# Kernel tuning notes

Hardware: AMD Instinct MI355X
Metric: run time of the kernel (lower is better)

Reference implementation:

```python
import jax, jax.numpy as jnp
import numpy as np

B, H, SQ, SKV, D = 4, 16, 2048, 2048, 128
SCALE = float(np.sqrt(D))  # scale_factor passed to forward; q_k is divided by it


def setup_inputs() -> dict:
    key = jax.random.key(0)
    kq, kk, kv = jax.random.split(key, 3)
    q = jax.random.normal(kq, (B, H, SQ, D), dtype=jnp.float32)
    k = jax.random.normal(kk, (B, H, SKV, D), dtype=jnp.float32)
    v = jax.random.normal(kv, (B, H, SKV, D), dtype=jnp.float32)
    return {"q": q, "k": k, "v": v}


def reference(q, k, v):
    # q_k = q @ k^T, divided by scale_factor
    scores = jnp.einsum("bhqd,bhkd->bhqk", q, k) / SCALE  # [B,H,Sq,Skv]
    attn = jax.nn.softmax(scores, axis=-1)
    # dropout(p=0.1) is identity in eval/inference mode
    out = jnp.einsum("bhqk,bhkd->bhqd", attn, v)  # [B,H,Sq,D]
    return out
```

## Files before the change

### kernel.cpp

```cpp
#include <hip/hip_runtime.h>
#include <hip/hip_bf16.h>

#define B_ 4
#define H_ 16
#define SQ 2048
#define SKV 2048
#define D_ 128
#define BH (B_*H_)
#define BM 128
#define BN 64
#define NITER (SKV/BN)

typedef __attribute__((ext_vector_type(8))) short bf16x8;
typedef __attribute__((ext_vector_type(4))) float f32x4;

__device__ inline unsigned short f2bf(float f) {
    union { float f; unsigned u; } x{f};
    unsigned r = x.u + 0x7fffu + ((x.u >> 16) & 1u);
    return (unsigned short)(r >> 16);
}

#if defined(__has_builtin) && __has_builtin(__builtin_amdgcn_cvt_pk_bf16_f32)
#define PKBF16(a,b) ({ auto _r = __builtin_amdgcn_cvt_pk_bf16_f32((a),(b)); \
                       unsigned _u; __builtin_memcpy(&_u, &_r, 4); _u; })
#else
#define PKBF16(a,b) ((unsigned)f2bf(a) | ((unsigned)f2bf(b) << 16))
#endif

__device__ inline void gl_lds16(const short* g, short* l) {
    __builtin_amdgcn_global_load_lds((const __attribute__((address_space(1))) unsigned*)g,
                                     (__attribute__((address_space(3))) unsigned*)l,
                                     16, 0, 0);
}

__global__ __launch_bounds__(256) void prep(const float* __restrict__ kin,
                                            const float* __restrict__ vin,
                                            short* __restrict__ kbf,
                                            short* __restrict__ vtg) {
    __shared__ short tile[64 * 136];
    int bx = blockIdx.x, tid = threadIdx.x;
    if (bx < 8192) {
        const float4* s = (const float4*)kin;
        uint2* d = (uint2*)kbf;
        int i = bx * 256 + tid;
        const int HALF = (BH * SKV * D_ / 4) / 2;
#pragma unroll
        for (int h = 0; h < 2; ++h) {
            int j = i + h * HALF;
            float4 a = s[j];
            d[j] = make_uint2(PKBF16(a.x, a.y), PKBF16(a.z, a.w));
        }
    } else {
        int bx2 = bx - 8192;
        int bh = bx2 >> 5;
        int t0 = (bx2 & 31) * 64;
        {
            int r = tid >> 4, cg = tid & 15;
#pragma unroll
            for (int s = 0; s < 4; ++s) {
                int rr = r + s * 16;
                const float* p = vin + ((size_t)bh * SKV + t0 + rr) * D_ + cg * 8;
                float4 a = *(const float4*)p;
                float4 b = *(const float4*)(p + 4);
                union { unsigned u[4]; bf16x8 v; } f;
                f.u[0] = PKBF16(a.x, a.y); f.u[1] = PKBF16(a.z, a.w);
                f.u[2] = PKBF16(b.x, b.y); f.u[3] = PKBF16(b.z, b.w);
                *(bf16x8*)&tile[rr * 136 + cg * 8] = f.v;
            }
        }
        __syncthreads();
        {
            int d = tid >> 1, h2 = tid & 1;
#pragma unroll
            for (int s = 0; s < 4; ++s) {
                int kv = h2 * 32 + s * 8;
                union { short u[8]; uint4 q; } o;
#pragma unroll
                for (int j = 0; j < 8; ++j) o.u[j] = tile[(kv + j) * 136 + d];
                *(uint4*)(vtg + ((size_t)bh * D_ + d) * SKV + t0 + kv) = o.q;
            }
        }
    }
}

__global__ __launch_bounds__(256, 3) void fa_kernel(const float* __restrict__ q,
                                                    const short* __restrict__ kbf,
                                                    const short* __restrict__ vtg,
                                                    float* __restrict__ out) {
    __shared__ short Ksh[64 * 128];
    __shared__ short Vsh[128 * 64];
    __shared__ short Psh[4 * 32 * 72];

    const int tid = threadIdx.x;
    const int wave = tid >> 6;
    const int lane = tid & 63;
    const int l16 = lane & 15;
    const int quad = lane >> 4;

    const int bx = blockIdx.x;
    const int qt = bx & 15;
    const int bh = bx >> 4;
    const int qrow0 = qt * BM + wave * 32;

    const float cscale = 1.4426950408889634f * 0.08838834764831845f;

    bf16x8 qf[2][4];
#pragma unroll
    for (int mt = 0; mt < 2; ++mt) {
        int row = qrow0 + mt * 16 + l16;
        const float* qp = q + ((size_t)bh * SQ + row) * D_ + quad * 8;
#pragma unroll
        for (int ks = 0; ks < 4; ++ks) {
            const float* p = qp + ks * 32;
            float4 a = *(const float4*)p;
            float4 b = *(const float4*)(p + 4);
            union { unsigned u[4]; bf16x8 v; } f;
            f.u[0] = PKBF16(a.x * cscale, a.y * cscale);
            f.u[1] = PKBF16(a.z * cscale, a.w * cscale);
            f.u[2] = PKBF16(b.x * cscale, b.y * cscale);
            f.u[3] = PKBF16(b.z * cscale, b.w * cscale);
            qf[mt][ks] = f.v;
        }
    }

    f32x4 oacc[8][2];
#pragma unroll
    for (int dt = 0; dt < 8; ++dt)
#pragma unroll
        for (int mt = 0; mt < 2; ++mt) oacc[dt][mt] = (f32x4)0.f;
    float lsum[2] = {0.f, 0.f};

    const short* kbase = kbf + (size_t)bh * SKV * D_;
    const short* vbase = vtg + (size_t)bh * D_ * SKV;
    const int krow0 = wave * 4 + (lane >> 4);
    const int kc8 = (lane & 15) ^ krow0;
    const short* kg = kbase + krow0 * 128 + kc8 * 8;
    short* kl = Ksh + wave * 512;
    const int vd0 = wave * 8 + (lane >> 3);
    const int vc = (lane & 7) ^ (lane >> 3);
    const short* vg = vbase + (size_t)vd0 * SKV + vc * 8;
    short* vl = Vsh + wave * 512;

    short* const pwav = Psh + wave * 2304;

    for (int it = 0; it < NITER; ++it) {
        __syncthreads();
#pragma unroll
        for (int s = 0; s < 4; ++s) {
            gl_lds16(kg + s * 2048, kl + s * 2048);
            gl_lds16(vg + (size_t)s * 32 * SKV, vl + s * 2048);
        }
        kg += BN * D_;
        vg += BN;
        __syncthreads();

        f32x4 sacc[4][2];
#pragma unroll
        for (int kt = 0; kt < 4; ++kt) {
            sacc[kt][0] = (f32x4)0.f; sacc[kt][1] = (f32x4)0.f;
        }
#pragma unroll
        for (int kt = 0; kt < 4; ++kt)
#pragma unroll
            for (int ks = 0; ks < 4; ++ks) {
                bf16x8 kf = *(const bf16x8*)&Ksh[(kt * 16 + l16) * 128 + (((ks * 4 + quad) ^ l16) << 3)];
                sacc[kt][0] = __builtin_amdgcn_mfma_f32_16x16x32_bf16(kf, qf[0][ks], sacc[kt][0], 0, 0, 0);
                sacc[kt][1] = __builtin_amdgcn_mfma_f32_16x16x32_bf16(kf, qf[1][ks], sacc[kt][1], 0, 0, 0);
            }

#pragma unroll
        for (int mt = 0; mt < 2; ++mt) {
            short* pw = pwav + (mt * 16 + l16) * 72;
#pragma unroll
            for (int kt = 0; kt < 4; ++kt) {
                float p0 = __builtin_amdgcn_exp2f(sacc[kt][mt][0]);
                float p1 = __builtin_amdgcn_exp2f(sacc[kt][mt][1]);
                float p2 = __builtin_amdgcn_exp2f(sacc[kt][mt][2]);
                float p3 = __builtin_amdgcn_exp2f(sacc[kt][mt][3]);
                lsum[mt] += (p0 + p1) + (p2 + p3);
                *(uint2*)(pw + kt * 16 + quad * 4) = make_uint2(PKBF16(p0, p1), PKBF16(p2, p3));
            }
        }

#pragma unroll
        for (int ks = 0; ks < 2; ++ks) {
            bf16x8 pa0 = *(const bf16x8*)(pwav + l16 * 72 + ks * 32 + quad * 8);
            bf16x8 pa1 = *(const bf16x8*)(pwav + (16 + l16) * 72 + ks * 32 + quad * 8);
#pragma unroll
            for (int dt = 0; dt < 8; ++dt) {
                bf16x8 vf = *(const bf16x8*)&Vsh[(dt * 16 + l16) * 64 + ((((ks * 4 + quad) ^ (l16 & 7))) << 3)];
                oacc[dt][0] = __builtin_amdgcn_mfma_f32_16x16x32_bf16(vf, pa0, oacc[dt][0], 0, 0, 0);
                oacc[dt][1] = __builtin_amdgcn_mfma_f32_16x16x32_bf16(vf, pa1, oacc[dt][1], 0, 0, 0);
            }
        }
    }

#pragma unroll
    for (int mt = 0; mt < 2; ++mt) {
        lsum[mt] += __shfl_xor(lsum[mt], 16);
        lsum[mt] += __shfl_xor(lsum[mt], 32);
    }
    const float rl[2] = {1.0f / lsum[0], 1.0f / lsum[1]};
#pragma unroll
    for (int mt = 0; mt < 2; ++mt) {
        float* op = out + ((size_t)bh * SQ + qrow0 + mt * 16 + l16) * D_ + quad * 4;
#pragma unroll
        for (int dt = 0; dt < 8; ++dt) {
            f32x4 v = oacc[dt][mt] * rl[mt];
            *(f32x4*)(op + dt * 16) = v;
        }
    }
}

extern "C" void kernel_launch(void* const* d_in, const int* in_sizes, int n_in,
                              void* d_out, int out_size, void* d_ws, size_t ws_size,
                              hipStream_t stream) {
    const float* q = (const float*)d_in[0];
    const float* k = (const float*)d_in[1];
    const float* v = (const float*)d_in[2];
    float* out = (float*)d_out;

    short* kbf = (short*)d_ws;
    short* vtg = kbf + (size_t)BH * SKV * D_;

    prep<<<8192 + 2048, 256, 0, stream>>>(k, v, kbf, vtg);
    fa_kernel<<<BH * (SQ / BM), 256, 0, stream>>>(q, kbf, vtg, out);
}
```

Baseline: 372.5 us.

## Double-buffer K/V tiles in LDS with BN=32 to overlap loads and MFMA

Halves the KV tile width to 32 and allocates two LDS buffers for K and V. The async global-to-LDS load of the next tile is issued before computing on the current one, so memory latency can overlap the QK^T, exp and PV MFMA work. The K/V address swizzles and the P scratch pitch are adapted to the narrower tile. The prep kernel's V transpose store also gets a new thread-to-data mapping. The cost is twice as many iterations and barriers per tile of work, plus fewer MFMAs between synchronisations.

```diff
diff --git a/kernel.cpp b/kernel.cpp
--- a/kernel.cpp
+++ b/kernel.cpp
@@ -8,7 +8,7 @@
 #define D_ 128
 #define BH (B_*H_)
 #define BM 128
-#define BN 64
+#define BN 32
 #define NITER (SKV/BN)
 
 typedef __attribute__((ext_vector_type(8))) short bf16x8;
@@ -70,14 +70,15 @@
         }
         __syncthreads();
         {
-            int d = tid >> 1, h2 = tid & 1;
+            int row = tid >> 3;
+            int c8 = tid & 7;
 #pragma unroll
             for (int s = 0; s < 4; ++s) {
-                int kv = h2 * 32 + s * 8;
+                int d = row + s * 32;
                 union { short u[8]; uint4 q; } o;
 #pragma unroll
-                for (int j = 0; j < 8; ++j) o.u[j] = tile[(kv + j) * 136 + d];
-                *(uint4*)(vtg + ((size_t)bh * D_ + d) * SKV + t0 + kv) = o.q;
+                for (int j = 0; j < 8; ++j) o.u[j] = tile[(c8 * 8 + j) * 136 + d];
+                *(uint4*)(vtg + ((size_t)bh * D_ + d) * SKV + t0 + c8 * 8) = o.q;
             }
         }
     }
@@ -87,9 +88,9 @@
                                                     const short* __restrict__ kbf,
                                                     const short* __restrict__ vtg,
                                                     float* __restrict__ out) {
-    __shared__ short Ksh[64 * 128];
-    __shared__ short Vsh[128 * 64];
-    __shared__ short Psh[4 * 32 * 72];
+    __shared__ short Ksh[2 * 32 * 128];
+    __shared__ short Vsh[2 * 128 * 32];
+    __shared__ short Psh[4 * 32 * 40];
 
     const int tid = threadIdx.x;
     const int wave = tid >> 6;
@@ -135,44 +136,41 @@
     const int krow0 = wave * 4 + (lane >> 4);
     const int kc8 = (lane & 15) ^ krow0;
     const short* kg = kbase + krow0 * 128 + kc8 * 8;
-    short* kl = Ksh + wave * 512;
-    const int vd0 = wave * 8 + (lane >> 3);
-    const int vc = (lane & 7) ^ (lane >> 3);
+    short* const klbase = Ksh + wave * 512;
+    const int vd0 = wave * 16 + (lane >> 2);
+    const int vc = (lane & 3) ^ ((lane >> 2) & 3);
     const short* vg = vbase + (size_t)vd0 * SKV + vc * 8;
-    short* vl = Vsh + wave * 512;
-
-    short* const pwav = Psh + wave * 2304;
-
-    for (int it = 0; it < NITER; ++it) {
-        __syncthreads();
-#pragma unroll
-        for (int s = 0; s < 4; ++s) {
-            gl_lds16(kg + s * 2048, kl + s * 2048);
-            gl_lds16(vg + (size_t)s * 32 * SKV, vl + s * 2048);
-        }
-        kg += BN * D_;
-        vg += BN;
-        __syncthreads();
-
-        f32x4 sacc[4][2];
-#pragma unroll
-        for (int kt = 0; kt < 4; ++kt) {
-            sacc[kt][0] = (f32x4)0.f; sacc[kt][1] = (f32x4)0.f;
-        }
-#pragma unroll
-        for (int kt = 0; kt < 4; ++kt)
+    short* const vlbase = Vsh + wave * 512;
+
+    short* const pwav = Psh + wave * 1280;
+
+    auto stage = [&](int it, int bufo) {
+        const short* kgi = kg + it * (BN * D_);
+        const short* vgi = vg + it * BN;
+#pragma unroll
+        for (int s = 0; s < 2; ++s) {
+            gl_lds16(kgi + s * 2048, klbase + bufo + s * 2048);
+            gl_lds16(vgi + (size_t)s * 64 * SKV, vlbase + bufo + s * 2048);
+        }
+    };
+
+    auto compute = [&](int bufo) {
+        f32x4 sacc[2][2];
+#pragma unroll
+        for (int kt = 0; kt < 2; ++kt) { sacc[kt][0] = (f32x4)0.f; sacc[kt][1] = (f32x4)0.f; }
+#pragma unroll
+        for (int kt = 0; kt < 2; ++kt)
 #pragma unroll
             for (int ks = 0; ks < 4; ++ks) {
-                bf16x8 kf = *(const bf16x8*)&Ksh[(kt * 16 + l16) * 128 + (((ks * 4 + quad) ^ l16) << 3)];
+                bf16x8 kf = *(const bf16x8*)&Ksh[bufo + (kt * 16 + l16) * 128 + (((ks * 4 + quad) ^ l16) << 3)];
                 sacc[kt][0] = __builtin_amdgcn_mfma_f32_16x16x32_bf16(kf, qf[0][ks], sacc[kt][0], 0, 0, 0);
                 sacc[kt][1] = __builtin_amdgcn_mfma_f32_16x16x32_bf16(kf, qf[1][ks], sacc[kt][1], 0, 0, 0);
             }
-
 #pragma unroll
         for (int mt = 0; mt < 2; ++mt) {
-            short* pw = pwav + (mt * 16 + l16) * 72;
-#pragma unroll
-            for (int kt = 0; kt < 4; ++kt) {
+            short* pw = pwav + (mt * 16 + l16) * 40;
+#pragma unroll
+            for (int kt = 0; kt < 2; ++kt) {
                 float p0 = __builtin_amdgcn_exp2f(sacc[kt][mt][0]);
                 float p1 = __builtin_amdgcn_exp2f(sacc[kt][mt][1]);
                 float p2 = __builtin_amdgcn_exp2f(sacc[kt][mt][2]);
@@ -181,18 +179,24 @@
                 *(uint2*)(pw + kt * 16 + quad * 4) = make_uint2(PKBF16(p0, p1), PKBF16(p2, p3));
             }
         }
-
-#pragma unroll
-        for (int ks = 0; ks < 2; ++ks) {
-            bf16x8 pa0 = *(const bf16x8*)(pwav + l16 * 72 + ks * 32 + quad * 8);
-            bf16x8 pa1 = *(const bf16x8*)(pwav + (16 + l16) * 72 + ks * 32 + quad * 8);
-#pragma unroll
-            for (int dt = 0; dt < 8; ++dt) {
-                bf16x8 vf = *(const bf16x8*)&Vsh[(dt * 16 + l16) * 64 + ((((ks * 4 + quad) ^ (l16 & 7))) << 3)];
-                oacc[dt][0] = __builtin_amdgcn_mfma_f32_16x16x32_bf16(vf, pa0, oacc[dt][0], 0, 0, 0);
-                oacc[dt][1] = __builtin_amdgcn_mfma_f32_16x16x32_bf16(vf, pa1, oacc[dt][1], 0, 0, 0);
-            }
-        }
+        bf16x8 pa0 = *(const bf16x8*)(pwav + l16 * 40 + quad * 8);
+        bf16x8 pa1 = *(const bf16x8*)(pwav + (16 + l16) * 40 + quad * 8);
+#pragma unroll
+        for (int dt = 0; dt < 8; ++dt) {
+            bf16x8 vf = *(const bf16x8*)&Vsh[bufo + (dt * 16 + l16) * 32 + ((quad ^ (l16 & 3)) << 3)];
+            oacc[dt][0] = __builtin_amdgcn_mfma_f32_16x16x32_bf16(vf, pa0, oacc[dt][0], 0, 0, 0);
+            oacc[dt][1] = __builtin_amdgcn_mfma_f32_16x16x32_bf16(vf, pa1, oacc[dt][1], 0, 0, 0);
+        }
+    };
+
+    stage(0, 0);
+    for (int it = 0; it < NITER; it += 2) {
+        __syncthreads();
+        stage(it + 1, 4096);
+        compute(0);
+        __syncthreads();
+        if (it + 2 < NITER) stage(it + 2, 0);
+        compute(4096);
     }
 
 #pragma unroll
```

New measurement: 380.6 us. 2.2% more time.
